# Kernel optimization log

Hardware: AMD Instinct MI355X
Metric: run time of the kernel (lower is better)

The kernel has to match this reference:

```python
import jax, jax.numpy as jnp
import numpy as np

EPS = 1e-12

def l2_normalize(x):
    # matches torch.nn.functional.normalize(p=2): x / max(||x||, eps)
    n = jnp.sqrt(jnp.sum(x * x, axis=-1, keepdims=True))
    return x / jnp.maximum(n, EPS)

def setup_inputs() -> dict:
    key = jax.random.key(0)
    k1, k2, k3, k4 = jax.random.split(key, 4)
    batch, n_neg, E, n_rel = 512, 2048, 256, 1000
    return {
        "head_emb": jax.random.normal(k1, (batch, E), dtype=jnp.float32),
        "tail_emb": jax.random.normal(k2, (1, n_neg, E), dtype=jnp.float32),
        "relation_embedding": jax.random.normal(k3, (n_rel, 2 * E), dtype=jnp.float32),
        "relation_id": jax.random.randint(k4, (batch,), 0, n_rel, dtype=jnp.int64),
    }

def reference(head_emb, tail_emb, relation_embedding, relation_id):
    # PairRE.score_tails with negative_sample_sharing=True, scoring_norm=2,
    # normalize_entities=True.
    E = head_emb.shape[-1]
    rel = relation_embedding[relation_id]          # (batch, 2E)
    r_h, r_t = rel[:, :E], rel[:, E:]              # (batch, E) each
    h = l2_normalize(head_emb)                     # (batch, E)
    t = l2_normalize(tail_emb)                     # (1, n_neg, E)
    t = t.reshape(1, -1, E)                        # negative sample sharing
    # diff: (batch, n_neg, E)
    diff = t * r_t[:, None, :] - (h * r_h)[:, None, :]
    # p=2 norm reduction over embedding dim -> (batch, n_neg)
    return -jnp.sqrt(jnp.sum(diff * diff, axis=-1))
```

## Files before the change

### kernel.cpp

```cpp
#include <hip/hip_runtime.h>
#include <hip/hip_bf16.h>


#define B_DIM 512
#define N_DIM 2048
#define E_DIM 256
#define LDA   520

typedef __attribute__((ext_vector_type(8))) __bf16 bf16x8;
typedef __attribute__((ext_vector_type(4))) float f32x4;

__device__ inline ushort f2bf(float x) {
    __hip_bfloat16 h = __float2bfloat16(x);
    union { __hip_bfloat16 b; ushort u; } cv; cv.b = h; return cv.u;
}

__device__ inline float wave_sum(float v) {
#pragma unroll
    for (int m = 1; m < 64; m <<= 1) v += __shfl_xor(v, m, 64);
    return v;
}

__global__ __launch_bounds__(256, 2) void pairre_one(
        const float* __restrict__ head, const float* __restrict__ tail,
        const float* __restrict__ rel,  const int* __restrict__ rid,
        float* __restrict__ out) {
    __shared__ ushort Alds[32 * LDA];
    __shared__ float cb_lds[32];

    const int tid = threadIdx.x, lane = tid & 63, wv = tid >> 6;
    const int ml = lane & 15, q = lane >> 4;
    const int bid = blockIdx.x;
    const int p_n = bid & 31, b_super = bid >> 5;

#pragma unroll
    for (int j = 0; j < 8; ++j) {
        const int rr = wv * 8 + j;
        const int b = b_super * 32 + rr;
        const int id = rid[b];
        const float4 h4  = *(const float4*)(head + (size_t)b * E_DIM + lane * 4);
        const float4 rh4 = *(const float4*)(rel + (size_t)id * 512 + lane * 4);
        const float4 rt4 = *(const float4*)(rel + (size_t)id * 512 + E_DIM + lane * 4);
        const float s1 = wave_sum(h4.x*h4.x + h4.y*h4.y + h4.z*h4.z + h4.w*h4.w);
        const float inv = 1.0f / fmaxf(sqrtf(s1), 1e-12f);
        const float p0 = h4.x*inv*rh4.x, p1 = h4.y*inv*rh4.y,
                    p2 = h4.z*inv*rh4.z, p3 = h4.w*inv*rh4.w;
        const float s2 = wave_sum(p0*p0 + p1*p1 + p2*p2 + p3*p3);
        if (lane == 0) cb_lds[rr] = s2;
        const ushort4 usq = { f2bf(rt4.x*rt4.x), f2bf(rt4.y*rt4.y),
                              f2bf(rt4.z*rt4.z), f2bf(rt4.w*rt4.w) };
        const ushort4 uli = { f2bf(-2.f*rt4.x*p0), f2bf(-2.f*rt4.y*p1),
                              f2bf(-2.f*rt4.z*p2), f2bf(-2.f*rt4.w*p3) };
        *(ushort4*)&Alds[rr * LDA + lane * 4] = usq;
        *(ushort4*)&Alds[rr * LDA + E_DIM + lane * 4] = uli;
    }
    __syncthreads();

    const int gT0 = p_n * 4 + (wv >> 1) * 2;
    const float* t0 = tail + (size_t)(gT0 * 16 + ml) * E_DIM + q * 8;
    const float* t1 = t0 + 16 * E_DIM;
    float a0 = 0.f, a1 = 0.f;
#pragma unroll
    for (int s = 0; s < 8; ++s) {
        const float4 x0 = *(const float4*)(t0 + s * 32);
        const float4 x1 = *(const float4*)(t0 + s * 32 + 4);
        const float4 y0 = *(const float4*)(t1 + s * 32);
        const float4 y1 = *(const float4*)(t1 + s * 32 + 4);
        a0 += x0.x*x0.x + x0.y*x0.y + x0.z*x0.z + x0.w*x0.w
            + x1.x*x1.x + x1.y*x1.y + x1.z*x1.z + x1.w*x1.w;
        a1 += y0.x*y0.x + y0.y*y0.y + y0.z*y0.z + y0.w*y0.w
            + y1.x*y1.x + y1.y*y1.y + y1.z*y1.z + y1.w*y1.w;
    }
    a0 += __shfl_xor(a0, 16, 64); a0 += __shfl_xor(a0, 32, 64);
    a1 += __shfl_xor(a1, 16, 64); a1 += __shfl_xor(a1, 32, 64);
    const float inv0 = 1.0f / fmaxf(sqrtf(a0), 1e-12f);
    const float inv1 = 1.0f / fmaxf(sqrtf(a1), 1e-12f);

    const ushort* Arow = &Alds[((wv & 1) * 16 + ml) * LDA];
    f32x4 acc0 = {0.f, 0.f, 0.f, 0.f}, acc1 = {0.f, 0.f, 0.f, 0.f};
#pragma unroll
    for (int s = 0; s < 8; ++s) {
        const float4 x0 = *(const float4*)(t0 + s * 32);
        const float4 x1 = *(const float4*)(t0 + s * 32 + 4);
        const float4 y0 = *(const float4*)(t1 + s * 32);
        const float4 y1 = *(const float4*)(t1 + s * 32 + 4);
        const float v0[8] = { x0.x*inv0, x0.y*inv0, x0.z*inv0, x0.w*inv0,
                              x1.x*inv0, x1.y*inv0, x1.z*inv0, x1.w*inv0 };
        const float v1[8] = { y0.x*inv1, y0.y*inv1, y0.z*inv1, y0.w*inv1,
                              y1.x*inv1, y1.y*inv1, y1.z*inv1, y1.w*inv1 };
        union { ushort u[8]; bf16x8 v; } sq0, li0, sq1, li1;
#pragma unroll
        for (int j = 0; j < 8; ++j) {
            sq0.u[j] = f2bf(v0[j] * v0[j]);  li0.u[j] = f2bf(v0[j]);
            sq1.u[j] = f2bf(v1[j] * v1[j]);  li1.u[j] = f2bf(v1[j]);
        }
        const bf16x8 a_lo = *(const bf16x8*)&Arow[s * 32 + q * 8];
        const bf16x8 a_hi = *(const bf16x8*)&Arow[E_DIM + s * 32 + q * 8];
        acc0 = __builtin_amdgcn_mfma_f32_16x16x32_bf16(a_lo, sq0.v, acc0, 0, 0, 0);
        acc0 = __builtin_amdgcn_mfma_f32_16x16x32_bf16(a_hi, li0.v, acc0, 0, 0, 0);
        acc1 = __builtin_amdgcn_mfma_f32_16x16x32_bf16(a_lo, sq1.v, acc1, 0, 0, 0);
        acc1 = __builtin_amdgcn_mfma_f32_16x16x32_bf16(a_hi, li1.v, acc1, 0, 0, 0);
    }

    const int n0 = gT0 * 16;
#pragma unroll
    for (int r = 0; r < 4; ++r) {
        const int rloc = (wv & 1) * 16 + q * 4 + r;
        const int b = b_super * 32 + rloc;
        const float cb = cb_lds[rloc];
        out[(size_t)b * N_DIM + n0 + ml]      = -sqrtf(fmaxf(acc0[r] + cb, 0.f));
        out[(size_t)b * N_DIM + n0 + 16 + ml] = -sqrtf(fmaxf(acc1[r] + cb, 0.f));
    }
}

extern "C" void kernel_launch(void* const* d_in, const int* in_sizes, int n_in,
                              void* d_out, int out_size, void* d_ws, size_t ws_size,
                              hipStream_t stream) {
    const float* head = (const float*)d_in[0];
    const float* tail = (const float*)d_in[1];
    const float* rel  = (const float*)d_in[2];
    const int*   rid  = (const int*)d_in[3];
    float* out = (float*)d_out;
    (void)d_ws; (void)ws_size;

    pairre_one<<<512, 256, 0, stream>>>(head, tail, rel, rid, out);
}
```

Baseline: 82.70 us.

## Retile to 32x32 output blocks with tail operands staged in LDS

Each block now covers a 32x32 output tile across 1024 blocks, instead of 32x64 across 512. Tail rows are loaded once, converted to bf16 square and linear operands, and stored in LDS in MFMA-fragment order. Tail normalization is moved out of the operands and applied in the epilogue, so the raw tail values go into the MFMA. This removes the doubled global reads of tail per wave and the per-wave conversion work, at the cost of smaller tiles, an extra __syncthreads, and redundant reloads of head and relation rows when building the A fragments.

```diff
diff --git a/kernel.cpp b/kernel.cpp
--- a/kernel.cpp
+++ b/kernel.cpp
@@ -5,7 +5,6 @@
 #define B_DIM 512
 #define N_DIM 2048
 #define E_DIM 256
-#define LDA   520
 
 typedef __attribute__((ext_vector_type(8))) __bf16 bf16x8;
 typedef __attribute__((ext_vector_type(4))) float f32x4;
@@ -21,95 +20,131 @@
     return v;
 }
 
-__global__ __launch_bounds__(256, 2) void pairre_one(
+__global__ __launch_bounds__(256) void pairre_single(
         const float* __restrict__ head, const float* __restrict__ tail,
         const float* __restrict__ rel,  const int* __restrict__ rid,
         float* __restrict__ out) {
-    __shared__ ushort Alds[32 * LDA];
-    __shared__ float cb_lds[32];
+    __shared__ ushort Alds[2 * 16 * 64 * 8];
+    __shared__ ushort Tsq[2 * 8 * 64 * 8];
+    __shared__ ushort Tli[2 * 8 * 64 * 8];
+    __shared__ float invh_s[32];
+    __shared__ float cb_s[32];
+    __shared__ float invt_s[32];
 
     const int tid = threadIdx.x, lane = tid & 63, wv = tid >> 6;
-    const int ml = lane & 15, q = lane >> 4;
     const int bid = blockIdx.x;
-    const int p_n = bid & 31, b_super = bid >> 5;
+    const int p_b = bid & 15, p_n = bid >> 4;
+    const int b0 = p_b * 32, n0 = p_n * 32;
 
 #pragma unroll
     for (int j = 0; j < 8; ++j) {
-        const int rr = wv * 8 + j;
-        const int b = b_super * 32 + rr;
+        const int rl = wv * 8 + j;
+        const int b = b0 + rl;
         const int id = rid[b];
-        const float4 h4  = *(const float4*)(head + (size_t)b * E_DIM + lane * 4);
-        const float4 rh4 = *(const float4*)(rel + (size_t)id * 512 + lane * 4);
-        const float4 rt4 = *(const float4*)(rel + (size_t)id * 512 + E_DIM + lane * 4);
+        const float4 h4 = *(const float4*)(head + (size_t)b * E_DIM + lane * 4);
+        const float4 r4 = *(const float4*)(rel + (size_t)id * 512 + lane * 4);
         const float s1 = wave_sum(h4.x*h4.x + h4.y*h4.y + h4.z*h4.z + h4.w*h4.w);
         const float inv = 1.0f / fmaxf(sqrtf(s1), 1e-12f);
-        const float p0 = h4.x*inv*rh4.x, p1 = h4.y*inv*rh4.y,
-                    p2 = h4.z*inv*rh4.z, p3 = h4.w*inv*rh4.w;
+        const float p0 = h4.x*inv*r4.x, p1 = h4.y*inv*r4.y,
+                    p2 = h4.z*inv*r4.z, p3 = h4.w*inv*r4.w;
         const float s2 = wave_sum(p0*p0 + p1*p1 + p2*p2 + p3*p3);
-        if (lane == 0) cb_lds[rr] = s2;
-        const ushort4 usq = { f2bf(rt4.x*rt4.x), f2bf(rt4.y*rt4.y),
-                              f2bf(rt4.z*rt4.z), f2bf(rt4.w*rt4.w) };
-        const ushort4 uli = { f2bf(-2.f*rt4.x*p0), f2bf(-2.f*rt4.y*p1),
-                              f2bf(-2.f*rt4.z*p2), f2bf(-2.f*rt4.w*p3) };
-        *(ushort4*)&Alds[rr * LDA + lane * 4] = usq;
-        *(ushort4*)&Alds[rr * LDA + E_DIM + lane * 4] = uli;
+        if (lane == 0) { invh_s[rl] = inv; cb_s[rl] = s2; }
+    }
+
+    {
+        const int q8 = lane & 7, roct = lane >> 3;
+        const int rloc = wv * 8 + roct;
+        const int grp = rloc >> 4, mloc = rloc & 15;
+        const float* trow = tail + (size_t)(n0 + rloc) * E_DIM;
+        float ss = 0.f;
+#pragma unroll
+        for (int s = 0; s < 4; ++s) {
+            const int c = s * 8 + q8;
+            const int e = c * 8;
+            const float4 a = *(const float4*)(trow + e);
+            const float4 b2 = *(const float4*)(trow + e + 4);
+            const float v[8] = {a.x,a.y,a.z,a.w,b2.x,b2.y,b2.z,b2.w};
+            ushort us[8], ul[8];
+#pragma unroll
+            for (int j = 0; j < 8; ++j) {
+                ss += v[j] * v[j];
+                us[j] = f2bf(v[j] * v[j]);
+                ul[j] = f2bf(v[j]);
+            }
+            const int s32 = c >> 2, q = c & 3, slot = q * 16 + mloc;
+            *(uint4*)&Tsq[((grp * 8 + s32) * 64 + slot) * 8] = *(const uint4*)us;
+            *(uint4*)&Tli[((grp * 8 + s32) * 64 + slot) * 8] = *(const uint4*)ul;
+        }
+        ss += __shfl_xor(ss, 1, 64);
+        ss += __shfl_xor(ss, 2, 64);
+        ss += __shfl_xor(ss, 4, 64);
+        if (q8 == 0) invt_s[rloc] = 1.0f / fmaxf(sqrtf(ss), 1e-12f);
     }
     __syncthreads();
 
-    const int gT0 = p_n * 4 + (wv >> 1) * 2;
-    const float* t0 = tail + (size_t)(gT0 * 16 + ml) * E_DIM + q * 8;
-    const float* t1 = t0 + 16 * E_DIM;
-    float a0 = 0.f, a1 = 0.f;
+#pragma unroll
+    for (int k = 0; k < 8; ++k) {
+        const int c = tid + k * 256;
+        const int gloc = c >> 10;
+        const int rem = c & 1023;
+        const int s = rem >> 6;
+        const int slot = rem & 63;
+        const int q = slot >> 4, mloc = slot & 15;
+        const int rl = gloc * 16 + mloc;
+        const int b = b0 + rl;
+        const int id = rid[b];
+        const float* rrow = rel + (size_t)id * 512;
+        float v[8];
+        if (s < 8) {
+            const int e = s * 32 + q * 8;
+            const float4 a = *(const float4*)(rrow + E_DIM + e);
+            const float4 bq = *(const float4*)(rrow + E_DIM + e + 4);
+            const float rt[8] = {a.x,a.y,a.z,a.w,bq.x,bq.y,bq.z,bq.w};
+#pragma unroll
+            for (int j = 0; j < 8; ++j) v[j] = rt[j] * rt[j];
+        } else {
+            const int e = (s - 8) * 32 + q * 8;
+            const float4 a = *(const float4*)(rrow + E_DIM + e);
+            const float4 bq = *(const float4*)(rrow + E_DIM + e + 4);
+            const float4 h0 = *(const float4*)(head + (size_t)b * E_DIM + e);
+            const float4 h1 = *(const float4*)(head + (size_t)b * E_DIM + e + 4);
+            const float4 r0 = *(const float4*)(rrow + e);
+            const float4 r1 = *(const float4*)(rrow + e + 4);
+            const float rt[8] = {a.x,a.y,a.z,a.w,bq.x,bq.y,bq.z,bq.w};
+            const float hh[8] = {h0.x,h0.y,h0.z,h0.w,h1.x,h1.y,h1.z,h1.w};
+            const float rr[8] = {r0.x,r0.y,r0.z,r0.w,r1.x,r1.y,r1.z,r1.w};
+            const float inv = invh_s[rl];
+#pragma unroll
+            for (int j = 0; j < 8; ++j) v[j] = -2.0f * rt[j] * (hh[j] * inv * rr[j]);
+        }
+        ushort u[8];
+#pragma unroll
+        for (int j = 0; j < 8; ++j) u[j] = f2bf(v[j]);
+        *(uint4*)&Alds[((gloc * 16 + s) * 64 + slot) * 8] = *(const uint4*)u;
+    }
+    __syncthreads();
+
+    const int wb = wv & 1, wn = wv >> 1;
+    f32x4 aS = {0.f,0.f,0.f,0.f}, aL = {0.f,0.f,0.f,0.f};
 #pragma unroll
     for (int s = 0; s < 8; ++s) {
-        const float4 x0 = *(const float4*)(t0 + s * 32);
-        const float4 x1 = *(const float4*)(t0 + s * 32 + 4);
-        const float4 y0 = *(const float4*)(t1 + s * 32);
-        const float4 y1 = *(const float4*)(t1 + s * 32 + 4);
-        a0 += x0.x*x0.x + x0.y*x0.y + x0.z*x0.z + x0.w*x0.w
-            + x1.x*x1.x + x1.y*x1.y + x1.z*x1.z + x1.w*x1.w;
-        a1 += y0.x*y0.x + y0.y*y0.y + y0.z*y0.z + y0.w*y0.w
-            + y1.x*y1.x + y1.y*y1.y + y1.z*y1.z + y1.w*y1.w;
-    }
-    a0 += __shfl_xor(a0, 16, 64); a0 += __shfl_xor(a0, 32, 64);
-    a1 += __shfl_xor(a1, 16, 64); a1 += __shfl_xor(a1, 32, 64);
-    const float inv0 = 1.0f / fmaxf(sqrtf(a0), 1e-12f);
-    const float inv1 = 1.0f / fmaxf(sqrtf(a1), 1e-12f);
-
-    const ushort* Arow = &Alds[((wv & 1) * 16 + ml) * LDA];
-    f32x4 acc0 = {0.f, 0.f, 0.f, 0.f}, acc1 = {0.f, 0.f, 0.f, 0.f};
-#pragma unroll
-    for (int s = 0; s < 8; ++s) {
-        const float4 x0 = *(const float4*)(t0 + s * 32);
-        const float4 x1 = *(const float4*)(t0 + s * 32 + 4);
-        const float4 y0 = *(const float4*)(t1 + s * 32);
-        const float4 y1 = *(const float4*)(t1 + s * 32 + 4);
-        const float v0[8] = { x0.x*inv0, x0.y*inv0, x0.z*inv0, x0.w*inv0,
-                              x1.x*inv0, x1.y*inv0, x1.z*inv0, x1.w*inv0 };
-        const float v1[8] = { y0.x*inv1, y0.y*inv1, y0.z*inv1, y0.w*inv1,
-                              y1.x*inv1, y1.y*inv1, y1.z*inv1, y1.w*inv1 };
-        union { ushort u[8]; bf16x8 v; } sq0, li0, sq1, li1;
-#pragma unroll
-        for (int j = 0; j < 8; ++j) {
-            sq0.u[j] = f2bf(v0[j] * v0[j]);  li0.u[j] = f2bf(v0[j]);
-            sq1.u[j] = f2bf(v1[j] * v1[j]);  li1.u[j] = f2bf(v1[j]);
-        }
-        const bf16x8 a_lo = *(const bf16x8*)&Arow[s * 32 + q * 8];
-        const bf16x8 a_hi = *(const bf16x8*)&Arow[E_DIM + s * 32 + q * 8];
-        acc0 = __builtin_amdgcn_mfma_f32_16x16x32_bf16(a_lo, sq0.v, acc0, 0, 0, 0);
-        acc0 = __builtin_amdgcn_mfma_f32_16x16x32_bf16(a_hi, li0.v, acc0, 0, 0, 0);
-        acc1 = __builtin_amdgcn_mfma_f32_16x16x32_bf16(a_lo, sq1.v, acc1, 0, 0, 0);
-        acc1 = __builtin_amdgcn_mfma_f32_16x16x32_bf16(a_hi, li1.v, acc1, 0, 0, 0);
+        const bf16x8 asq = *(const bf16x8*)&Alds[((wb * 16 + s) * 64 + lane) * 8];
+        const bf16x8 ali = *(const bf16x8*)&Alds[((wb * 16 + 8 + s) * 64 + lane) * 8];
+        const bf16x8 tq  = *(const bf16x8*)&Tsq[((wn * 8 + s) * 64 + lane) * 8];
+        const bf16x8 tl  = *(const bf16x8*)&Tli[((wn * 8 + s) * 64 + lane) * 8];
+        aS = __builtin_amdgcn_mfma_f32_16x16x32_bf16(asq, tq, aS, 0, 0, 0);
+        aL = __builtin_amdgcn_mfma_f32_16x16x32_bf16(ali, tl, aL, 0, 0, 0);
     }
 
-    const int n0 = gT0 * 16;
+    const int ml = lane & 15, q = lane >> 4;
+    const float it = invt_s[wn * 16 + ml];
+    const int nn = n0 + wn * 16 + ml;
 #pragma unroll
     for (int r = 0; r < 4; ++r) {
-        const int rloc = (wv & 1) * 16 + q * 4 + r;
-        const int b = b_super * 32 + rloc;
-        const float cb = cb_lds[rloc];
-        out[(size_t)b * N_DIM + n0 + ml]      = -sqrtf(fmaxf(acc0[r] + cb, 0.f));
-        out[(size_t)b * N_DIM + n0 + 16 + ml] = -sqrtf(fmaxf(acc1[r] + cb, 0.f));
+        const int rl = wb * 16 + q * 4 + r;
+        const int b = b0 + rl;
+        const float x = aS[r] * it * it + aL[r] * it + cb_s[rl];
+        out[(size_t)b * N_DIM + nn] = -sqrtf(fmaxf(x, 0.f));
     }
 }
 
@@ -123,5 +158,5 @@
     float* out = (float*)d_out;
     (void)d_ws; (void)ws_size;
 
-    pairre_one<<<512, 256, 0, stream>>>(head, tail, rel, rid, out);
+    pairre_single<<<1024, 256, 0, stream>>>(head, tail, rel, rid, out);
 }
```

Measured after the change: 93.88 us. 1.14x slower.
